# Performance work log

Hardware: AMD Instinct MI355X
Metric: run time of the kernel (lower is better)

Reference implementation:

```python
import jax, jax.numpy as jnp
import numpy as np

ALPHA = 0.2   # leaky relu negative slope
EPS = 1e-5    # layernorm eps
NEG = -1e12   # mask value from original code


def gat_layer(x, adj, W, a):
    # x: [N, F_in], adj: [N, N] bool, W: [F_in, F_out], a: [2*F_out, 1]
    F_out = W.shape[1]
    Wh = x @ W                                  # [N, F_out]
    # a^T [Wh_i ; Wh_j] decomposes into f1_i + f2_j (same math as the
    # O(N^2 * 2F) concat in the torch code, without materializing it)
    f1 = Wh @ a[:F_out]                         # [N, 1]
    f2 = Wh @ a[F_out:]                         # [N, 1]
    e = jax.nn.leaky_relu(f1 + f2.T, negative_slope=ALPHA)  # [N, N]
    att = jnp.where(adj, e, NEG)
    att = jax.nn.softmax(att, axis=1)           # dropout p=0.0 -> no-op
    return att @ Wh                             # [N, F_out]


def layernorm(x, g, b):
    mu = jnp.mean(x, axis=-1, keepdims=True)
    var = jnp.var(x, axis=-1, keepdims=True)
    return (x - mu) * jax.lax.rsqrt(var + EPS) * g + b


def setup_inputs() -> dict:
    N, F = 8192, 128
    key = jax.random.key(0)
    ks = jax.random.split(key, 12)
    inp = {
        "input_hs": jax.random.normal(ks[0], (2, N, F), jnp.float32),
        "adjs": jax.random.uniform(ks[1], (2, N, N)) < 0.3,   # bool adjacency
        "MPNN_emb": jax.random.normal(ks[2], (N, F), jnp.float32),
        "query": jax.random.normal(ks[3], (1, F), jnp.float32),
        # learned params (xavier-ish scale)
        "W0": jax.random.normal(ks[4], (F, F), jnp.float32) * (1.414 / np.sqrt(F)),
        "a0": jax.random.normal(ks[5], (2 * F, 1), jnp.float32) * 0.1,
        "W1": jax.random.normal(ks[6], (F, F), jnp.float32) * (1.414 / np.sqrt(F)),
        "a1": jax.random.normal(ks[7], (2 * F, 1), jnp.float32) * 0.1,
        "ln_gamma": jnp.ones((F,), jnp.float32),
        "ln_beta": jnp.zeros((F,), jnp.float32),
        "res": jax.random.normal(ks[8], (1, 1), jnp.float32) * 0.5,
    }
    return inp


def reference(input_hs, adjs, MPNN_emb, query, W0, a0, W1, a1, ln_gamma, ln_beta, res):
    h0 = gat_layer(input_hs[0], adjs[0], W0, a0)   # [N, F]
    h1 = gat_layer(input_hs[1], adjs[1], W1, a1)   # [N, F]
    q = layernorm(query, ln_gamma, ln_beta)        # [1, F]
    w1 = q @ h0.T                                  # [1, N]
    w2 = q @ h1.T
    w3 = q @ MPNN_emb.T
    scores = jax.nn.softmax(jnp.concatenate([w1, w2, w3], axis=0), axis=0)  # [3, N]
    # diag_embed(s) @ H is just per-row scaling s[:, None] * H
    mix = (scores[0][:, None] * h0
           + scores[1][:, None] * h1
           + scores[2][:, None] * MPNN_emb)
    return res * mix + input_hs[0]
```

## Files before the change

### kernel.cpp

```cpp
#include <hip/hip_runtime.h>
#include <hip/hip_bf16.h>
#include <cstdint>


#define N 8192
#define F 128
#define JS 4
#define RT 128
#define PSTR 40

typedef __attribute__((ext_vector_type(8))) short short8;
typedef __attribute__((ext_vector_type(8))) unsigned short ushort8;
typedef __attribute__((ext_vector_type(4))) float floatx4;

__device__ inline unsigned short f2bf(float x) {
  unsigned int u = __float_as_uint(x);
  u += 0x7FFFu + ((u >> 16) & 1u);
  return (unsigned short)(u >> 16);
}


__global__ __launch_bounds__(128) void k1_wh(
    const float* __restrict__ X2, const float* __restrict__ W0,
    const float* __restrict__ W1, const float* __restrict__ a0,
    const float* __restrict__ a1, unsigned short* __restrict__ Whbt,
    float* __restrict__ f1g, float* __restrict__ f2g) {
  const int l  = blockIdx.y;
  const int i0 = blockIdx.x * 16;
  const int c  = threadIdx.x;
  const float* __restrict__ X = X2 + (size_t)l * N * F + (size_t)i0 * F;
  const float* __restrict__ W = l ? W1 : W0;

  __shared__ __align__(16) float sX[16 * F];
  __shared__ float red[2][2][16];
  {
    const float4* src = (const float4*)X;
    float4* dst = (float4*)sX;
#pragma unroll
    for (int qq = 0; qq < 4; ++qq) dst[qq * 128 + c] = src[qq * 128 + c];
  }
  __syncthreads();

  float acc[16];
#pragma unroll
  for (int r = 0; r < 16; ++r) acc[r] = 0.f;

  for (int f4 = 0; f4 < 32; ++f4) {
    float w0 = W[(f4 * 4 + 0) * F + c];
    float w1 = W[(f4 * 4 + 1) * F + c];
    float w2 = W[(f4 * 4 + 2) * F + c];
    float w3 = W[(f4 * 4 + 3) * F + c];
#pragma unroll
    for (int r = 0; r < 16; ++r) {
      float4 xv = *(const float4*)(&sX[r * F + f4 * 4]);
      acc[r] = fmaf(xv.x, w0, acc[r]);
      acc[r] = fmaf(xv.y, w1, acc[r]);
      acc[r] = fmaf(xv.z, w2, acc[r]);
      acc[r] = fmaf(xv.w, w3, acc[r]);
    }
  }

  {
    unsigned short* wdst = Whbt + (size_t)l * F * N + (size_t)c * N + i0;
    ushort8 u0, u1;
#pragma unroll
    for (int r = 0; r < 8; ++r) {
      u0[r] = f2bf(acc[r]);
      u1[r] = f2bf(acc[8 + r]);
    }
    *(ushort8*)wdst = u0;
    *(ushort8*)(wdst + 8) = u1;
  }

  const float* __restrict__ a = l ? a1 : a0;
  const float a1c = a[c], a2c = a[F + c];
  const int w = c >> 6, lane = c & 63;
#pragma unroll
  for (int r = 0; r < 16; ++r) {
    float s1 = acc[r] * a1c;
    float s2 = acc[r] * a2c;
#pragma unroll
    for (int off = 32; off; off >>= 1) {
      s1 += __shfl_down(s1, off);
      s2 += __shfl_down(s2, off);
    }
    if (lane == 0) {
      red[w][0][r] = s1;
      red[w][1][r] = s2;
    }
  }
  __syncthreads();
  if (c < 16)
    f1g[l * N + i0 + c] = red[0][0][c] + red[1][0][c];
  else if (c < 32)
    f2g[l * N + i0 + c - 16] = red[0][1][c - 16] + red[1][1][c - 16];
}

__global__ __launch_bounds__(128) void k3_qln(
    const float* __restrict__ query, const float* __restrict__ gamma,
    const float* __restrict__ beta, float* __restrict__ qln) {
  const int t = threadIdx.x;
  float v = query[t];
  float s = v, sq = v * v;
#pragma unroll
  for (int off = 32; off; off >>= 1) {
    s += __shfl_down(s, off);
    sq += __shfl_down(sq, off);
  }
  __shared__ float sb[4];
  if ((t & 63) == 0) {
    sb[t >> 6] = s;
    sb[2 + (t >> 6)] = sq;
  }
  __syncthreads();
  float S = sb[0] + sb[1], SQ = sb[2] + sb[3];
  float mu = S * (1.f / 128.f);
  float var = SQ * (1.f / 128.f) - mu * mu;
  qln[t] = (v - mu) * rsqrtf(var + 1e-5f) * gamma[t] + beta[t];
}

__global__ __launch_bounds__(256) void k2_attn(
    const unsigned short* __restrict__ Whbt, const float* __restrict__ f1g,
    const float* __restrict__ f2g, const int* __restrict__ adj,
    float* __restrict__ hpart, float* __restrict__ Lpart) {
  const int l  = blockIdx.y;
  const int s  = blockIdx.z;
  const int i0 = blockIdx.x * RT;
  const int t  = threadIdx.x;
  const int wave = t >> 6;
  const int lane = t & 63;
  const int lpos = lane & 15;
  const int halfk = lane >> 4;

  const int q  = t & 7;
  const int r0 = t >> 3;

  __shared__ __align__(16) unsigned short sP[RT * PSTR];
  __shared__ __align__(16) unsigned short sB[F * PSTR];

  const unsigned short* __restrict__ WhbL = Whbt + (size_t)l * F * N;
  const int* __restrict__ adjL = adj + (size_t)l * N * N;
  const float* __restrict__ f2L = f2g + l * N;

  float f1v[4];
  const int* adjR[4];
#pragma unroll
  for (int rp = 0; rp < 4; ++rp) {
    f1v[rp] = f1g[l * N + i0 + r0 + 32 * rp];
    adjR[rp] = adjL + (size_t)(i0 + r0 + 32 * rp) * N;
  }
  const unsigned short* wsrc0 = WhbL + (size_t)(t >> 1) * N + (t & 1) * 16;
  const int sBoff = (t >> 1) * PSTR + (t & 1) * 16;

  floatx4 acc[2][9];
#pragma unroll
  for (int mt = 0; mt < 2; ++mt)
#pragma unroll
    for (int nt = 0; nt < 9; ++nt) acc[mt][nt] = (floatx4){0.f, 0.f, 0.f, 0.f};

  short8 ones;
  {
    short v = (lpos == 0) ? (short)0x3F80 : (short)0;
#pragma unroll
    for (int e = 0; e < 8; ++e) ones[e] = v;
  }

  const int jbeg = s * (N / JS), jend = (s + 1) * (N / JS);
  for (int j0 = jbeg; j0 < jend; j0 += 32) {
    uint4 wv0 = *(const uint4*)(wsrc0 + j0);
    uint4 wv1 = *(const uint4*)(wsrc0 + j0 + 8);
    float4 f2v = *(const float4*)(f2L + j0 + 4 * q);
    int4 av[4];
#pragma unroll
    for (int rp = 0; rp < 4; ++rp) av[rp] = *(const int4*)(adjR[rp] + j0 + 4 * q);

    uint2 pk[4];
#pragma unroll
    for (int rp = 0; rp < 4; ++rp) {
      float b = f1v[rp];
      float s0 = b + f2v.x, s1 = b + f2v.y, s2 = b + f2v.z, s3 = b + f2v.w;
      s0 = fmaxf(s0, 0.2f * s0);
      s1 = fmaxf(s1, 0.2f * s1);
      s2 = fmaxf(s2, 0.2f * s2);
      s3 = fmaxf(s3, 0.2f * s3);
      float p0 = av[rp].x ? __expf(s0) : 0.f;
      float p1 = av[rp].y ? __expf(s1) : 0.f;
      float p2 = av[rp].z ? __expf(s2) : 0.f;
      float p3 = av[rp].w ? __expf(s3) : 0.f;
      pk[rp].x = (unsigned int)f2bf(p0) | ((unsigned int)f2bf(p1) << 16);
      pk[rp].y = (unsigned int)f2bf(p2) | ((unsigned int)f2bf(p3) << 16);
    }

    __syncthreads();
    *(uint4*)&sB[sBoff] = wv0;
    *(uint4*)&sB[sBoff + 8] = wv1;
#pragma unroll
    for (int rp = 0; rp < 4; ++rp)
      *(uint2*)&sP[(r0 + 32 * rp) * PSTR + 4 * q] = pk[rp];
    __syncthreads();

    short8 af[2];
#pragma unroll
    for (int mt = 0; mt < 2; ++mt)
      af[mt] = *(const short8*)&sP[(wave * 32 + mt * 16 + lpos) * PSTR + halfk * 8];
#pragma unroll
    for (int nt = 0; nt < 8; ++nt) {
      short8 bf = *(const short8*)&sB[(nt * 16 + lpos) * PSTR + halfk * 8];
      acc[0][nt] = __builtin_amdgcn_mfma_f32_16x16x32_bf16(af[0], bf, acc[0][nt], 0, 0, 0);
      acc[1][nt] = __builtin_amdgcn_mfma_f32_16x16x32_bf16(af[1], bf, acc[1][nt], 0, 0, 0);
    }
    acc[0][8] = __builtin_amdgcn_mfma_f32_16x16x32_bf16(af[0], ones, acc[0][8], 0, 0, 0);
    acc[1][8] = __builtin_amdgcn_mfma_f32_16x16x32_bf16(af[1], ones, acc[1][8], 0, 0, 0);
  }

  const size_t obase = ((size_t)(l * JS + s) * N + i0) * F;
  const size_t lbase = (size_t)(l * JS + s) * N + i0;
#pragma unroll
  for (int mt = 0; mt < 2; ++mt) {
    const int rb = wave * 32 + mt * 16 + halfk * 4;
#pragma unroll
    for (int nt = 0; nt < 8; ++nt) {
#pragma unroll
      for (int reg = 0; reg < 4; ++reg)
        hpart[obase + (size_t)(rb + reg) * F + nt * 16 + lpos] = acc[mt][nt][reg];
    }
    if (lpos == 0) {
#pragma unroll
      for (int reg = 0; reg < 4; ++reg)
        Lpart[lbase + rb + reg] = acc[mt][8][reg];
    }
  }
}

__global__ __launch_bounds__(256) void k4_mix(
    const float* __restrict__ hpart, const float* __restrict__ Lpart,
    const float* __restrict__ MPNN, const float* __restrict__ qln,
    const float* __restrict__ x0, const float* __restrict__ res,
    float* __restrict__ out) {
  const int row  = blockIdx.x * 4 + (threadIdx.x >> 6);
  const int lane = threadIdx.x & 63;
  const int c    = lane * 2;

  float h0x = 0.f, h0y = 0.f, h1x = 0.f, h1y = 0.f, L0 = 0.f, L1 = 0.f;
#pragma unroll
  for (int sx = 0; sx < JS; ++sx) {
    float2 v0 = *(const float2*)&hpart[((size_t)(0 * JS + sx) * N + row) * F + c];
    float2 v1 = *(const float2*)&hpart[((size_t)(1 * JS + sx) * N + row) * F + c];
    h0x += v0.x; h0y += v0.y;
    h1x += v1.x; h1y += v1.y;
    L0 += Lpart[(size_t)(0 * JS + sx) * N + row];
    L1 += Lpart[(size_t)(1 * JS + sx) * N + row];
  }
  const float i0v = 1.f / L0, i1v = 1.f / L1;
  h0x *= i0v; h0y *= i0v;
  h1x *= i1v; h1y *= i1v;

  float2 mv = *(const float2*)&MPNN[(size_t)row * F + c];
  float2 qv = *(const float2*)&qln[c];
  float w1 = qv.x * h0x + qv.y * h0y;
  float w2 = qv.x * h1x + qv.y * h1y;
  float w3 = qv.x * mv.x + qv.y * mv.y;
#pragma unroll
  for (int off = 1; off < 64; off <<= 1) {
    w1 += __shfl_xor(w1, off);
    w2 += __shfl_xor(w2, off);
    w3 += __shfl_xor(w3, off);
  }
  float m = fmaxf(w1, fmaxf(w2, w3));
  float e1 = __expf(w1 - m), e2 = __expf(w2 - m), e3 = __expf(w3 - m);
  float inv = res[0] / (e1 + e2 + e3);
  float2 xr = *(const float2*)&x0[(size_t)row * F + c];
  float2 o;
  o.x = (e1 * h0x + e2 * h1x + e3 * mv.x) * inv + xr.x;
  o.y = (e1 * h0y + e2 * h1y + e3 * mv.y) * inv + xr.y;
  *(float2*)&out[(size_t)row * F + c] = o;
}

extern "C" void kernel_launch(void* const* d_in, const int* in_sizes, int n_in,
                              void* d_out, int out_size, void* d_ws,
                              size_t ws_size, hipStream_t stream) {
  const float* x2    = (const float*)d_in[0];
  const int*   adj   = (const int*)d_in[1];
  const float* mpnn  = (const float*)d_in[2];
  const float* query = (const float*)d_in[3];
  const float* W0    = (const float*)d_in[4];
  const float* a0    = (const float*)d_in[5];
  const float* W1    = (const float*)d_in[6];
  const float* a1    = (const float*)d_in[7];
  const float* gamma = (const float*)d_in[8];
  const float* beta  = (const float*)d_in[9];
  const float* res   = (const float*)d_in[10];

  float* ws = (float*)d_ws;
  unsigned short* Whbt = (unsigned short*)ws;
  float* hpart = ws + 1048576;
  float* f1g   = ws + 9437184;
  float* f2g   = ws + 9453568;
  float* Lpart = ws + 9469952;
  float* qln   = ws + 9535488;
  float* out   = (float*)d_out;

  k1_wh<<<dim3(N / 16, 2), 128, 0, stream>>>(x2, W0, W1, a0, a1, Whbt, f1g, f2g);
  k3_qln<<<1, 128, 0, stream>>>(query, gamma, beta, qln);
  k2_attn<<<dim3(N / RT, 2, JS), 256, 0, stream>>>(Whbt, f1g, f2g, adj, hpart,
                                                   Lpart);
  k4_mix<<<N / 4, 256, 0, stream>>>(hpart, Lpart, mpnn, qln, x2, res, out);
}
```

Baseline: 783.9 us.

## Compute attention fragments directly in MFMA registers, drop LDS staging, split J eightfold

```diff
diff --git a/kernel.cpp b/kernel.cpp
--- a/kernel.cpp
+++ b/kernel.cpp
@@ -5,18 +5,16 @@
 
 #define N 8192
 #define F 128
-#define JS 4
-#define RT 128
-#define PSTR 40
+#define JS 8
 
 typedef __attribute__((ext_vector_type(8))) short short8;
 typedef __attribute__((ext_vector_type(8))) unsigned short ushort8;
 typedef __attribute__((ext_vector_type(4))) float floatx4;
 
-__device__ inline unsigned short f2bf(float x) {
+__device__ inline unsigned int f2bf(float x) {
   unsigned int u = __float_as_uint(x);
   u += 0x7FFFu + ((u >> 16) & 1u);
-  return (unsigned short)(u >> 16);
+  return u >> 16;
 }
 
 
@@ -65,8 +63,8 @@
     ushort8 u0, u1;
 #pragma unroll
     for (int r = 0; r < 8; ++r) {
-      u0[r] = f2bf(acc[r]);
-      u1[r] = f2bf(acc[8 + r]);
+      u0[r] = (unsigned short)f2bf(acc[r]);
+      u1[r] = (unsigned short)f2bf(acc[8 + r]);
     }
     *(ushort8*)wdst = u0;
     *(ushort8*)(wdst + 8) = u1;
@@ -119,98 +117,79 @@
   qln[t] = (v - mu) * rsqrtf(var + 1e-5f) * gamma[t] + beta[t];
 }
 
+__device__ inline short8 make_pfrag(float f1v, const float4& fa,
+                                    const float4& fb, const int4& a0,
+                                    const int4& a1, float& Lacc) {
+  float p0, p1, p2, p3, p4, p5, p6, p7, sc;
+  sc = f1v + fa.x; sc = fmaxf(sc, 0.2f * sc); p0 = a0.x ? __expf(sc) : 0.f;
+  sc = f1v + fa.y; sc = fmaxf(sc, 0.2f * sc); p1 = a0.y ? __expf(sc) : 0.f;
+  sc = f1v + fa.z; sc = fmaxf(sc, 0.2f * sc); p2 = a0.z ? __expf(sc) : 0.f;
+  sc = f1v + fa.w; sc = fmaxf(sc, 0.2f * sc); p3 = a0.w ? __expf(sc) : 0.f;
+  sc = f1v + fb.x; sc = fmaxf(sc, 0.2f * sc); p4 = a1.x ? __expf(sc) : 0.f;
+  sc = f1v + fb.y; sc = fmaxf(sc, 0.2f * sc); p5 = a1.y ? __expf(sc) : 0.f;
+  sc = f1v + fb.z; sc = fmaxf(sc, 0.2f * sc); p6 = a1.z ? __expf(sc) : 0.f;
+  sc = f1v + fb.w; sc = fmaxf(sc, 0.2f * sc); p7 = a1.w ? __expf(sc) : 0.f;
+  Lacc += ((p0 + p1) + (p2 + p3)) + ((p4 + p5) + (p6 + p7));
+  union { unsigned int u[4]; short8 s8; } r;
+  r.u[0] = f2bf(p0) | (f2bf(p1) << 16);
+  r.u[1] = f2bf(p2) | (f2bf(p3) << 16);
+  r.u[2] = f2bf(p4) | (f2bf(p5) << 16);
+  r.u[3] = f2bf(p6) | (f2bf(p7) << 16);
+  return r.s8;
+}
+
 __global__ __launch_bounds__(256) void k2_attn(
     const unsigned short* __restrict__ Whbt, const float* __restrict__ f1g,
     const float* __restrict__ f2g, const int* __restrict__ adj,
     float* __restrict__ hpart, float* __restrict__ Lpart) {
   const int l  = blockIdx.y;
   const int s  = blockIdx.z;
-  const int i0 = blockIdx.x * RT;
+  const int i0 = blockIdx.x * 128;
   const int t  = threadIdx.x;
-  const int wave = t >> 6;
-  const int lane = t & 63;
-  const int lpos = lane & 15;
-  const int halfk = lane >> 4;
-
-  const int q  = t & 7;
-  const int r0 = t >> 3;
-
-  __shared__ __align__(16) unsigned short sP[RT * PSTR];
-  __shared__ __align__(16) unsigned short sB[F * PSTR];
+  const int wave = t >> 6, lane = t & 63;
+  const int lpos = lane & 15, halfk = lane >> 4;
 
   const unsigned short* __restrict__ WhbL = Whbt + (size_t)l * F * N;
   const int* __restrict__ adjL = adj + (size_t)l * N * N;
   const float* __restrict__ f2L = f2g + l * N;
 
-  float f1v[4];
-  const int* adjR[4];
-#pragma unroll
-  for (int rp = 0; rp < 4; ++rp) {
-    f1v[rp] = f1g[l * N + i0 + r0 + 32 * rp];
-    adjR[rp] = adjL + (size_t)(i0 + r0 + 32 * rp) * N;
-  }
-  const unsigned short* wsrc0 = WhbL + (size_t)(t >> 1) * N + (t & 1) * 16;
-  const int sBoff = (t >> 1) * PSTR + (t & 1) * 16;
-
-  floatx4 acc[2][9];
+  const int rowA = i0 + wave * 32 + lpos;
+  const float f1a = f1g[l * N + rowA];
+  const float f1b = f1g[l * N + rowA + 16];
+  const int* __restrict__ adjA = adjL + (size_t)rowA * N + halfk * 8;
+  const int* __restrict__ adjB = adjA + (size_t)16 * N;
+  const unsigned short* __restrict__ bbase = WhbL + (size_t)lpos * N + halfk * 8;
+  const float* __restrict__ f2base = f2L + halfk * 8;
+
+  floatx4 acc[2][8];
 #pragma unroll
   for (int mt = 0; mt < 2; ++mt)
 #pragma unroll
-    for (int nt = 0; nt < 9; ++nt) acc[mt][nt] = (floatx4){0.f, 0.f, 0.f, 0.f};
-
-  short8 ones;
-  {
-    short v = (lpos == 0) ? (short)0x3F80 : (short)0;
-#pragma unroll
-    for (int e = 0; e < 8; ++e) ones[e] = v;
-  }
-
-  const int jbeg = s * (N / JS), jend = (s + 1) * (N / JS);
-  for (int j0 = jbeg; j0 < jend; j0 += 32) {
-    uint4 wv0 = *(const uint4*)(wsrc0 + j0);
-    uint4 wv1 = *(const uint4*)(wsrc0 + j0 + 8);
-    float4 f2v = *(const float4*)(f2L + j0 + 4 * q);
-    int4 av[4];
-#pragma unroll
-    for (int rp = 0; rp < 4; ++rp) av[rp] = *(const int4*)(adjR[rp] + j0 + 4 * q);
-
-    uint2 pk[4];
-#pragma unroll
-    for (int rp = 0; rp < 4; ++rp) {
-      float b = f1v[rp];
-      float s0 = b + f2v.x, s1 = b + f2v.y, s2 = b + f2v.z, s3 = b + f2v.w;
-      s0 = fmaxf(s0, 0.2f * s0);
-      s1 = fmaxf(s1, 0.2f * s1);
-      s2 = fmaxf(s2, 0.2f * s2);
-      s3 = fmaxf(s3, 0.2f * s3);
-      float p0 = av[rp].x ? __expf(s0) : 0.f;
-      float p1 = av[rp].y ? __expf(s1) : 0.f;
-      float p2 = av[rp].z ? __expf(s2) : 0.f;
-      float p3 = av[rp].w ? __expf(s3) : 0.f;
-      pk[rp].x = (unsigned int)f2bf(p0) | ((unsigned int)f2bf(p1) << 16);
-      pk[rp].y = (unsigned int)f2bf(p2) | ((unsigned int)f2bf(p3) << 16);
-    }
-
-    __syncthreads();
-    *(uint4*)&sB[sBoff] = wv0;
-    *(uint4*)&sB[sBoff + 8] = wv1;
-#pragma unroll
-    for (int rp = 0; rp < 4; ++rp)
-      *(uint2*)&sP[(r0 + 32 * rp) * PSTR + 4 * q] = pk[rp];
-    __syncthreads();
-
-    short8 af[2];
-#pragma unroll
-    for (int mt = 0; mt < 2; ++mt)
-      af[mt] = *(const short8*)&sP[(wave * 32 + mt * 16 + lpos) * PSTR + halfk * 8];
+    for (int nt = 0; nt < 8; ++nt) acc[mt][nt] = (floatx4){0.f, 0.f, 0.f, 0.f};
+  float Lacc0 = 0.f, Lacc1 = 0.f;
+
+  const int jbeg = s * (N / JS);
+  for (int jj = 0; jj < N / JS; jj += 32) {
+    const int j0 = jbeg + jj;
+    int4 a0 = *(const int4*)(adjA + j0);
+    int4 a1 = *(const int4*)(adjA + j0 + 4);
+    int4 b0 = *(const int4*)(adjB + j0);
+    int4 b1 = *(const int4*)(adjB + j0 + 4);
+    float4 fa = *(const float4*)(f2base + j0);
+    float4 fb = *(const float4*)(f2base + j0 + 4);
+    short8 bfv[8];
+#pragma unroll
+    for (int nt = 0; nt < 8; ++nt)
+      bfv[nt] = *(const short8*)(bbase + (size_t)nt * 16 * N + j0);
+
+    short8 af0 = make_pfrag(f1a, fa, fb, a0, a1, Lacc0);
+    short8 af1 = make_pfrag(f1b, fa, fb, b0, b1, Lacc1);
+
 #pragma unroll
     for (int nt = 0; nt < 8; ++nt) {
-      short8 bf = *(const short8*)&sB[(nt * 16 + lpos) * PSTR + halfk * 8];
-      acc[0][nt] = __builtin_amdgcn_mfma_f32_16x16x32_bf16(af[0], bf, acc[0][nt], 0, 0, 0);
-      acc[1][nt] = __builtin_amdgcn_mfma_f32_16x16x32_bf16(af[1], bf, acc[1][nt], 0, 0, 0);
-    }
-    acc[0][8] = __builtin_amdgcn_mfma_f32_16x16x32_bf16(af[0], ones, acc[0][8], 0, 0, 0);
-    acc[1][8] = __builtin_amdgcn_mfma_f32_16x16x32_bf16(af[1], ones, acc[1][8], 0, 0, 0);
+      acc[0][nt] = __builtin_amdgcn_mfma_f32_16x16x32_bf16(af0, bfv[nt], acc[0][nt], 0, 0, 0);
+      acc[1][nt] = __builtin_amdgcn_mfma_f32_16x16x32_bf16(af1, bfv[nt], acc[1][nt], 0, 0, 0);
+    }
   }
 
   const size_t obase = ((size_t)(l * JS + s) * N + i0) * F;
@@ -224,11 +203,14 @@
       for (int reg = 0; reg < 4; ++reg)
         hpart[obase + (size_t)(rb + reg) * F + nt * 16 + lpos] = acc[mt][nt][reg];
     }
-    if (lpos == 0) {
-#pragma unroll
-      for (int reg = 0; reg < 4; ++reg)
-        Lpart[lbase + rb + reg] = acc[mt][8][reg];
-    }
+  }
+  Lacc0 += __shfl_xor(Lacc0, 16);
+  Lacc0 += __shfl_xor(Lacc0, 32);
+  Lacc1 += __shfl_xor(Lacc1, 16);
+  Lacc1 += __shfl_xor(Lacc1, 32);
+  if (halfk == 0) {
+    Lpart[lbase + wave * 32 + lpos] = Lacc0;
+    Lpart[lbase + wave * 32 + 16 + lpos] = Lacc1;
   }
 }
 
@@ -294,15 +276,15 @@
   float* ws = (float*)d_ws;
   unsigned short* Whbt = (unsigned short*)ws;
   float* hpart = ws + 1048576;
-  float* f1g   = ws + 9437184;
-  float* f2g   = ws + 9453568;
-  float* Lpart = ws + 9469952;
-  float* qln   = ws + 9535488;
+  float* f1g   = ws + 17825792;
+  float* f2g   = ws + 17842176;
+  float* Lpart = ws + 17858560;
+  float* qln   = ws + 17989632;
   float* out   = (float*)d_out;
 
   k1_wh<<<dim3(N / 16, 2), 128, 0, stream>>>(x2, W0, W1, a0, a1, Whbt, f1g, f2g);
   k3_qln<<<1, 128, 0, stream>>>(query, gamma, beta, qln);
-  k2_attn<<<dim3(N / RT, 2, JS), 256, 0, stream>>>(Whbt, f1g, f2g, adj, hpart,
-                                                   Lpart);
+  k2_attn<<<dim3(N / 128, 2, JS), 256, 0, stream>>>(Whbt, f1g, f2g, adj, hpart,
+                                                    Lpart);
   k4_mix<<<N / 4, 256, 0, stream>>>(hpart, Lpart, mpnn, qln, x2, res, out);
 }
```

Result: slower. 836.4 us (+6.7%).
